# Kernel tuning notes

Hardware: AMD Instinct MI355X
Metric: run time of the kernel (lower is better)

The kernel has to match this reference:

```python
import jax, jax.numpy as jnp
import numpy as np

B, S, D, H = 2, 2048, 1024, 16
DK = D // H

def setup_inputs() -> dict:
    key = jax.random.key(0)
    ks = jax.random.split(key, 12)
    sc = 0.02
    return {
        "q": jax.random.normal(ks[0], (B, S, D), jnp.float32),
        "k": jax.random.normal(ks[1], (B, S, D), jnp.float32),
        "v": jax.random.normal(ks[2], (B, S, D), jnp.float32),
        "mask": jnp.ones((1, 1, S, S), jnp.int32),
        "w_q": jax.random.normal(ks[3], (D, D), jnp.float32) * sc,
        "b_q": jnp.zeros((D,), jnp.float32),
        "w_k": jax.random.normal(ks[4], (D, D), jnp.float32) * sc,
        "b_k": jnp.zeros((D,), jnp.float32),
        "w_v": jax.random.normal(ks[5], (D, D), jnp.float32) * sc,
        "b_v": jnp.zeros((D,), jnp.float32),
        "w_o": jax.random.normal(ks[6], (D, D), jnp.float32) * sc,
        "b_o": jnp.zeros((D,), jnp.float32),
    }

def reference(q, k, v, mask, w_q, b_q, w_k, b_k, w_v, b_v, w_o, b_o):
    # torch Linear: y = x @ W.T + b, W is [out, in]
    def lin(x, w, b):
        return jnp.einsum('bsd,ed->bse', x, w) + b
    # project and split heads -> [B, H, S, DK]
    def heads(x):
        return x.reshape(B, S, H, DK).transpose(0, 2, 1, 3)
    Q = heads(lin(q, w_q, b_q))
    K = heads(lin(k, w_k, b_k))
    V = heads(lin(v, w_v, b_v))
    scores = jnp.einsum('bhqd,bhkd->bhqk', Q, K) / jnp.sqrt(jnp.float32(DK))
    scores = jnp.where(mask == 0, jnp.float32(-1e9), scores)
    attn = jax.nn.softmax(scores, axis=-1)  # dropout p=0 -> identity
    ctx = jnp.einsum('bhqk,bhkd->bhqd', attn, V)
    ctx = ctx.transpose(0, 2, 1, 3).reshape(B, S, D)
    return lin(ctx, w_o, b_o)
```

## Files before the change

kernel.cpp:

```cpp
#include <hip/hip_runtime.h>
#include <stdint.h>


#define S_LEN 2048
#define LOG2E 1.4426950408889634f

using bf16x8 = __attribute__((ext_vector_type(8))) __bf16;
using f32x4 = __attribute__((ext_vector_type(4))) float;
using f32x16 = __attribute__((ext_vector_type(16))) float;
using u32x4 = __attribute__((ext_vector_type(4))) unsigned int;

__device__ __forceinline__ unsigned short f2bf(float x) {
  unsigned int u = __builtin_bit_cast(unsigned int, x);
  u += 0x7fffu + ((u >> 16) & 1u);
  return (unsigned short)(u >> 16);
}

__device__ __forceinline__ void gload_lds16(const void* g, void* l) {
  __builtin_amdgcn_global_load_lds(
      (const __attribute__((address_space(1))) void*)g,
      (__attribute__((address_space(3))) void*)l, 16, 0, 0);
}

__device__ __forceinline__ unsigned int cvtpk(float lo, float hi) {
  unsigned int r;
  asm("v_cvt_pk_bf16_f32 %0, %1, %2" : "=v"(r) : "v"(lo), "v"(hi));
  return r;
}

__device__ __forceinline__ bf16x8 mkfrag(float p0, float p1, float p2, float p3,
                                         float p4, float p5, float p6, float p7) {
  auto r02 = __builtin_amdgcn_permlane32_swap(cvtpk(p0, p1), cvtpk(p4, p5),
                                              false, false);
  auto r13 = __builtin_amdgcn_permlane32_swap(cvtpk(p2, p3), cvtpk(p6, p7),
                                              false, false);
  u32x4 w = {(unsigned int)r02[0], (unsigned int)r13[0], (unsigned int)r02[1],
             (unsigned int)r13[1]};
  return __builtin_bit_cast(bf16x8, w);
}

__global__ void cvt4_kernel(const float* __restrict__ s0,
                            const float* __restrict__ s1,
                            const float* __restrict__ s2,
                            const float* __restrict__ s3,
                            unsigned short* __restrict__ d0,
                            unsigned short* __restrict__ d1,
                            unsigned short* __restrict__ d2,
                            unsigned short* __restrict__ d3, int n4) {
  const int which = blockIdx.y;
  const float* src = which == 0 ? s0 : which == 1 ? s1 : which == 2 ? s2 : s3;
  unsigned short* dst = which == 0 ? d0 : which == 1 ? d1 : which == 2 ? d2 : d3;
  int i = blockIdx.x * blockDim.x + threadIdx.x;
  int stride = gridDim.x * blockDim.x;
  for (; i < n4; i += stride) {
    float4 v = ((const float4*)src)[i];
    ushort4 o;
    o.x = f2bf(v.x);
    o.y = f2bf(v.y);
    o.z = f2bf(v.z);
    o.w = f2bf(v.w);
    ((ushort4*)dst)[i] = o;
  }
}

template <bool SWAP>
__device__ __forceinline__ void qkv_body(const float* __restrict__ X,
                                         const unsigned short* __restrict__ W,
                                         const float* __restrict__ bias,
                                         unsigned short* __restrict__ dst,
                                         float scale) {
  __shared__ unsigned short As[64 * 32];
  __shared__ unsigned short Bs[128 * 32];
  const int tid = threadIdx.x;
  const int wid = tid >> 6;
  const int lane = tid & 63;
  const int l15 = lane & 15, lg = lane >> 4;
  const int bm = blockIdx.y * 64;
  const int bn = blockIdx.x * 128;
  const int wr = (wid >> 1) * 32;
  const int wc = (wid & 1) * 64;

  const f32x4 fz = {0.f, 0.f, 0.f, 0.f};
  f32x4 acc[2][4];
#pragma unroll
  for (int m = 0; m < 2; ++m)
#pragma unroll
    for (int n = 0; n < 4; ++n) acc[m][n] = fz;

  const int ar = tid >> 2, ac = (tid & 3) * 8;
  const float* Ag = X + (size_t)(bm + ar) * 1024 + ac;
  const int srow = lane >> 2, scol = (lane & 3) * 8;

  for (int kt = 0; kt < 1024; kt += 32) {
    float4 a0 = *(const float4*)(Ag + kt);
    float4 a1 = *(const float4*)(Ag + kt + 4);
    u32x4 ap = {cvtpk(a0.x, a0.y), cvtpk(a0.z, a0.w), cvtpk(a1.x, a1.y),
                cvtpk(a1.z, a1.w)};
    *(u32x4*)&As[ar * 32 + ac] = ap;
#pragma unroll
    for (int c = 0; c < 2; ++c) {
      int ch = wid * 2 + c;
      gload_lds16(W + (size_t)(bn + ch * 16 + srow) * 1024 + kt + scol,
                  Bs + ch * 512);
    }
    __syncthreads();

    bf16x8 af[2], bfr[4];
#pragma unroll
    for (int m = 0; m < 2; ++m)
      af[m] = *(const bf16x8*)&As[(wr + m * 16 + l15) * 32 + lg * 8];
#pragma unroll
    for (int n = 0; n < 4; ++n)
      bfr[n] = *(const bf16x8*)&Bs[(wc + n * 16 + l15) * 32 + lg * 8];

#pragma unroll
    for (int m = 0; m < 2; ++m)
#pragma unroll
      for (int n = 0; n < 4; ++n) {
        if (SWAP)
          acc[m][n] = __builtin_amdgcn_mfma_f32_16x16x32_bf16(
              bfr[n], af[m], acc[m][n], 0, 0, 0);
        else
          acc[m][n] = __builtin_amdgcn_mfma_f32_16x16x32_bf16(
              af[m], bfr[n], acc[m][n], 0, 0, 0);
      }
    __syncthreads();
  }

#pragma unroll
  for (int m = 0; m < 2; ++m)
#pragma unroll
    for (int n = 0; n < 4; ++n)
#pragma unroll
      for (int j = 0; j < 4; ++j) {
        float a = acc[m][n][j];
        if (SWAP) {
          int gn = bn + wc + n * 16 + lg * 4 + j;
          int gm = bm + wr + m * 16 + l15;
          float v = a + bias[gn];
          int b = gm >> 11, s = gm & 2047;
          int h = gn >> 6, dk = gn & 63;
          dst[(((size_t)(b * 16 + h)) * 64 + dk) * 2048 + s] = f2bf(v);
        } else {
          int gm = bm + wr + m * 16 + lg * 4 + j;
          int gn = bn + wc + n * 16 + l15;
          float v = (a + bias[gn]) * scale;
          int b = gm >> 11, s = gm & 2047;
          int h = gn >> 6, dk = gn & 63;
          dst[(((size_t)(b * 16 + h)) * 2048 + s) * 64 + dk] = f2bf(v);
        }
      }
}

__global__ __launch_bounds__(256) void gemm_qkv(
    const float* __restrict__ X0, const float* __restrict__ X1,
    const float* __restrict__ X2, const unsigned short* __restrict__ W0,
    const unsigned short* __restrict__ W1,
    const unsigned short* __restrict__ W2, const float* __restrict__ b0,
    const float* __restrict__ b1, const float* __restrict__ b2,
    unsigned short* __restrict__ dq, unsigned short* __restrict__ dk,
    unsigned short* __restrict__ dv) {
  const int z = blockIdx.z;
  if (z == 0)
    qkv_body<false>(X0, W0, b0, dq, 0.125f * LOG2E);
  else if (z == 1)
    qkv_body<false>(X1, W1, b1, dk, 1.0f);
  else
    qkv_body<true>(X2, W2, b2, dv, 1.0f);
}

__global__ __launch_bounds__(256) void gemm_out(
    const unsigned short* __restrict__ X, const unsigned short* __restrict__ W,
    const float* __restrict__ bias, float* __restrict__ dstF) {
  __shared__ unsigned short As[64 * 32];
  __shared__ unsigned short Bs[128 * 32];
  const int tid = threadIdx.x;
  const int wid = tid >> 6;
  const int lane = tid & 63;
  const int l15 = lane & 15, lg = lane >> 4;
  const int bm = blockIdx.y * 64;
  const int bn = blockIdx.x * 128;
  const int wr = (wid >> 1) * 32;
  const int wc = (wid & 1) * 64;

  const f32x4 fz = {0.f, 0.f, 0.f, 0.f};
  f32x4 acc[2][4];
#pragma unroll
  for (int m = 0; m < 2; ++m)
#pragma unroll
    for (int n = 0; n < 4; ++n) acc[m][n] = fz;

  const int srow = lane >> 2, scol = (lane & 3) * 8;

  for (int kt = 0; kt < 1024; kt += 32) {
    gload_lds16(X + (size_t)(bm + wid * 16 + srow) * 1024 + kt + scol,
                As + wid * 512);
#pragma unroll
    for (int c = 0; c < 2; ++c) {
      int ch = wid * 2 + c;
      gload_lds16(W + (size_t)(bn + ch * 16 + srow) * 1024 + kt + scol,
                  Bs + ch * 512);
    }
    __syncthreads();

    bf16x8 af[2], bfr[4];
#pragma unroll
    for (int m = 0; m < 2; ++m)
      af[m] = *(const bf16x8*)&As[(wr + m * 16 + l15) * 32 + lg * 8];
#pragma unroll
    for (int n = 0; n < 4; ++n)
      bfr[n] = *(const bf16x8*)&Bs[(wc + n * 16 + l15) * 32 + lg * 8];

#pragma unroll
    for (int m = 0; m < 2; ++m)
#pragma unroll
      for (int n = 0; n < 4; ++n)
        acc[m][n] = __builtin_amdgcn_mfma_f32_16x16x32_bf16(af[m], bfr[n],
                                                            acc[m][n], 0, 0, 0);
    __syncthreads();
  }

#pragma unroll
  for (int m = 0; m < 2; ++m)
#pragma unroll
    for (int n = 0; n < 4; ++n)
#pragma unroll
      for (int j = 0; j < 4; ++j) {
        int gm = bm + wr + m * 16 + lg * 4 + j;
        int gn = bn + wc + n * 16 + l15;
        dstF[(size_t)gm * 1024 + gn] = acc[m][n][j] + bias[gn];
      }
}

__global__ __launch_bounds__(256) void attn_kernel(
    const unsigned short* __restrict__ Q,
    const unsigned short* __restrict__ K,
    const unsigned short* __restrict__ VT,
    unsigned short* __restrict__ CTX) {
  const int orig = blockIdx.x;
  const int wg = (orig & 7) * 64 + (orig >> 3);
  const int bh = wg >> 4;
  const int qb = wg & 15;
  const int tid = threadIdx.x;
  const int w = tid >> 6;
  const int lane = tid & 63;
  const int l31 = lane & 31;
  const int hi = lane >> 5;
  const int q0 = qb * 128 + w * 32;

  __shared__ __align__(16) unsigned short Ks[3][64][64];
  __shared__ __align__(16) unsigned short Vs[3][64][64];
  __shared__ float ls[4][32];

  const unsigned short* Qg = Q + ((size_t)bh * S_LEN + q0) * 64;
  const unsigned short* Kg = K + (size_t)bh * S_LEN * 64;
  const unsigned short* Vg = VT + (size_t)bh * 64 * S_LEN;

  bf16x8 qf[4];
#pragma unroll
  for (int kc = 0; kc < 4; ++kc)
    qf[kc] = *(const bf16x8*)&Qg[l31 * 64 + kc * 16 + hi * 8];

  const int srow = lane >> 3;
  const int sslot = (lane & 7) ^ srow;

#define STAGE(buf, kt)                                                         \
  {                                                                            \
    gload_lds16(Kg + ((size_t)((kt) + w * 16 + srow)) * 64 + sslot * 8,        \
                &Ks[buf][w * 16][0]);                                          \
    gload_lds16(Kg + ((size_t)((kt) + w * 16 + 8 + srow)) * 64 + sslot * 8,    \
                &Ks[buf][w * 16 + 8][0]);                                      \
    gload_lds16(Vg + ((size_t)(w * 16 + srow)) * S_LEN + (kt) + sslot * 8,     \
                &Vs[buf][w * 16][0]);                                          \
    gload_lds16(Vg + ((size_t)(w * 16 + 8 + srow)) * S_LEN + (kt) + sslot * 8, \
                &Vs[buf][w * 16 + 8][0]);                                      \
  }

  f32x16 O0 = {}, O1 = {};
  float m = -1e30f, lsum = 0.f;

  STAGE(0, 0)
  STAGE(1, 64)
  int cur = 0;

  for (int t = 0; t < 32; ++t) {
    if (t < 31) {
      asm volatile("s_waitcnt vmcnt(4)\n\ts_barrier" ::: "memory");
    } else {
      asm volatile("s_waitcnt vmcnt(0)\n\ts_barrier" ::: "memory");
    }
    if (t < 30) {
      int nb = cur >= 1 ? cur - 1 : cur + 2;
      STAGE(nb, (t + 2) * 64)
    }

    f32x16 s0 = {}, s1 = {};
    __builtin_amdgcn_s_setprio(1);
#pragma unroll
    for (int kc = 0; kc < 4; ++kc) {
      const int col = ((kc * 2 + hi) ^ (l31 & 7)) * 8;
      bf16x8 kf0 = *(const bf16x8*)&Ks[cur][l31][col];
      bf16x8 kf1 = *(const bf16x8*)&Ks[cur][32 + l31][col];
      s0 = __builtin_amdgcn_mfma_f32_32x32x16_bf16(kf0, qf[kc], s0, 0, 0, 0);
      s1 = __builtin_amdgcn_mfma_f32_32x32x16_bf16(kf1, qf[kc], s1, 0, 0, 0);
    }
    __builtin_amdgcn_s_setprio(0);

    float tmax[8];
#pragma unroll
    for (int i = 0; i < 8; ++i)
      tmax[i] = fmaxf(fmaxf(s0[i], s0[i + 8]), fmaxf(s1[i], s1[i + 8]));
    float pm = fmaxf(fmaxf(fmaxf(tmax[0], tmax[1]), fmaxf(tmax[2], tmax[3])),
                     fmaxf(fmaxf(tmax[4], tmax[5]), fmaxf(tmax[6], tmax[7])));
    pm = fmaxf(pm, __shfl_xor(pm, 32, 64));

    if (!__all(pm - m <= 8.0f)) {
      float mn = fmaxf(m, pm);
      float al = exp2f(m - mn);
      m = mn;
      lsum *= al;
      ls[w][l31] = al;
#pragma unroll
      for (int r = 0; r < 16; ++r) {
        float a = ls[w][(r & 3) + 8 * (r >> 2) + 4 * hi];
        O0[r] *= a;
        O1[r] *= a;
      }
    }

#pragma unroll
    for (int r = 0; r < 16; ++r) {
      s0[r] = exp2f(s0[r] - m);
      s1[r] = exp2f(s1[r] - m);
    }
    float sa = 0.f, sb = 0.f, sc = 0.f, sd = 0.f;
#pragma unroll
    for (int r = 0; r < 4; ++r) {
      sa += s0[r];
      sb += s0[r + 4];
      sc += s0[r + 8];
      sd += s0[r + 12];
      sa += s1[r];
      sb += s1[r + 4];
      sc += s1[r + 8];
      sd += s1[r + 12];
    }
    float ts = (sa + sb) + (sc + sd);
    ts += __shfl_xor(ts, 32, 64);
    lsum += ts;

    bf16x8 pa0 = mkfrag(s0[0], s0[1], s0[2], s0[3], s0[4], s0[5], s0[6], s0[7]);
    bf16x8 pa1 =
        mkfrag(s0[8], s0[9], s0[10], s0[11], s0[12], s0[13], s0[14], s0[15]);
    bf16x8 pa2 = mkfrag(s1[0], s1[1], s1[2], s1[3], s1[4], s1[5], s1[6], s1[7]);
    bf16x8 pa3 =
        mkfrag(s1[8], s1[9], s1[10], s1[11], s1[12], s1[13], s1[14], s1[15]);

    __builtin_amdgcn_s_setprio(1);
#pragma unroll
    for (int kc = 0; kc < 4; ++kc) {
      const int col = ((kc * 2 + hi) ^ (l31 & 7)) * 8;
      bf16x8 v0 = *(const bf16x8*)&Vs[cur][l31][col];
      bf16x8 v1 = *(const bf16x8*)&Vs[cur][32 + l31][col];
      bf16x8 pa = (kc == 0) ? pa0 : (kc == 1) ? pa1 : (kc == 2) ? pa2 : pa3;
      O0 = __builtin_amdgcn_mfma_f32_32x32x16_bf16(pa, v0, O0, 0, 0, 0);
      O1 = __builtin_amdgcn_mfma_f32_32x32x16_bf16(pa, v1, O1, 0, 0, 0);
    }
    __builtin_amdgcn_s_setprio(0);

    cur = cur == 2 ? 0 : cur + 1;
  }

  ls[w][l31] = lsum;
  const int b = bh >> 4, h = bh & 15;
#pragma unroll
  for (int r = 0; r < 16; ++r) {
    int qr = (r & 3) + 8 * (r >> 2) + 4 * hi;
    float inv = __builtin_amdgcn_rcpf(ls[w][qr]);
    size_t base = ((size_t)b * S_LEN + q0 + qr) * 1024 + h * 64;
    CTX[base + l31] = f2bf(O0[r] * inv);
    CTX[base + 32 + l31] = f2bf(O1[r] * inv);
  }
#undef STAGE
}

extern "C" void kernel_launch(void* const* d_in, const int* in_sizes, int n_in,
                              void* d_out, int out_size, void* d_ws,
                              size_t ws_size, hipStream_t stream) {
  const float* q = (const float*)d_in[0];
  const float* k = (const float*)d_in[1];
  const float* v = (const float*)d_in[2];
  const float* wq = (const float*)d_in[4];
  const float* bq = (const float*)d_in[5];
  const float* wk = (const float*)d_in[6];
  const float* bk = (const float*)d_in[7];
  const float* wv = (const float*)d_in[8];
  const float* bv = (const float*)d_in[9];
  const float* wo = (const float*)d_in[10];
  const float* bo = (const float*)d_in[11];
  float* out = (float*)d_out;

  const size_t NTOK = 4096 * 1024;
  unsigned short* ws = (unsigned short*)d_ws;
  unsigned short* wqb = ws;
  unsigned short* wkb = wqb + 1048576;
  unsigned short* wvb = wkb + 1048576;
  unsigned short* wob = wvb + 1048576;
  unsigned short* Qp = wob + 1048576;
  unsigned short* Kp = Qp + NTOK;
  unsigned short* Vt = Kp + NTOK;
  unsigned short* CTX = Vt + NTOK;

  cvt4_kernel<<<dim3(256, 4), 256, 0, stream>>>(wq, wk, wv, wo, wqb, wkb, wvb,
                                                wob, 262144);

  gemm_qkv<<<dim3(8, 64, 3), 256, 0, stream>>>(q, k, v, wqb, wkb, wvb, bq, bk,
                                               bv, Qp, Kp, Vt);

  attn_kernel<<<512, 256, 0, stream>>>(Qp, Kp, Vt, CTX);

  gemm_out<<<dim3(8, 64), 256, 0, stream>>>(CTX, wob, bo, out);
}
```

Measured before the change: 166.9 us.

## Enlarge GEMM tiles to 128x128 and remap blocks per XCD for L2 locality

Both projection GEMMs now share one templated body with 128x128 output tiles, with each wave computing 64x64 (4x4 MFMA fragments) instead of 32x64. This halves the block count and doubles the A-tile reuse per loaded B tile. Block indices are also remapped so each XCD handles contiguous row panels, keeping weight and activation tiles resident in that XCD's L2. The trade-off is more accumulator registers per thread and fewer blocks in flight (768 and 256), which lowers occupancy and can hurt latency hiding in the single-buffered loop.

After: 172.8 us. 3.6% more time.

```diff
diff --git a/kernel.cpp b/kernel.cpp
--- a/kernel.cpp
+++ b/kernel.cpp
@@ -63,40 +63,51 @@
   }
 }
 
-template <bool SWAP>
-__device__ __forceinline__ void qkv_body(const float* __restrict__ X,
-                                         const unsigned short* __restrict__ W,
-                                         const float* __restrict__ bias,
-                                         unsigned short* __restrict__ dst,
-                                         float scale) {
-  __shared__ unsigned short As[64 * 32];
+template <int APATH, int OMODE>
+__device__ __forceinline__ void gemm128_body(
+    const void* Xv, const unsigned short* __restrict__ W,
+    const float* __restrict__ bias, unsigned short* __restrict__ dstB,
+    float* __restrict__ dstF, float scale, int tx, int ty) {
+  __shared__ unsigned short As[128 * 32];
   __shared__ unsigned short Bs[128 * 32];
   const int tid = threadIdx.x;
-  const int wid = tid >> 6;
-  const int lane = tid & 63;
+  const int wid = tid >> 6, lane = tid & 63;
   const int l15 = lane & 15, lg = lane >> 4;
-  const int bm = blockIdx.y * 64;
-  const int bn = blockIdx.x * 128;
-  const int wr = (wid >> 1) * 32;
-  const int wc = (wid & 1) * 64;
+  const int bm = ty * 128, bn = tx * 128;
+  const int wr = (wid >> 1) * 64, wc = (wid & 1) * 64;
 
   const f32x4 fz = {0.f, 0.f, 0.f, 0.f};
-  f32x4 acc[2][4];
-#pragma unroll
-  for (int m = 0; m < 2; ++m)
+  f32x4 acc[4][4];
+#pragma unroll
+  for (int m = 0; m < 4; ++m)
 #pragma unroll
     for (int n = 0; n < 4; ++n) acc[m][n] = fz;
 
-  const int ar = tid >> 2, ac = (tid & 3) * 8;
-  const float* Ag = X + (size_t)(bm + ar) * 1024 + ac;
   const int srow = lane >> 2, scol = (lane & 3) * 8;
+  const int ar = tid >> 1, ac = (tid & 1) * 16;
+  const float* Af = (const float*)Xv + (size_t)(bm + ar) * 1024 + ac;
+  const unsigned short* Ab = (const unsigned short*)Xv;
 
   for (int kt = 0; kt < 1024; kt += 32) {
-    float4 a0 = *(const float4*)(Ag + kt);
-    float4 a1 = *(const float4*)(Ag + kt + 4);
-    u32x4 ap = {cvtpk(a0.x, a0.y), cvtpk(a0.z, a0.w), cvtpk(a1.x, a1.y),
-                cvtpk(a1.z, a1.w)};
-    *(u32x4*)&As[ar * 32 + ac] = ap;
+    if (APATH == 0) {
+      float4 a0 = *(const float4*)(Af + kt);
+      float4 a1 = *(const float4*)(Af + kt + 4);
+      float4 a2 = *(const float4*)(Af + kt + 8);
+      float4 a3 = *(const float4*)(Af + kt + 12);
+      u32x4 p0 = {cvtpk(a0.x, a0.y), cvtpk(a0.z, a0.w), cvtpk(a1.x, a1.y),
+                  cvtpk(a1.z, a1.w)};
+      u32x4 p1 = {cvtpk(a2.x, a2.y), cvtpk(a2.z, a2.w), cvtpk(a3.x, a3.y),
+                  cvtpk(a3.z, a3.w)};
+      *(u32x4*)&As[ar * 32 + ac] = p0;
+      *(u32x4*)&As[ar * 32 + ac + 8] = p1;
+    } else {
+#pragma unroll
+      for (int c = 0; c < 2; ++c) {
+        int ch = wid * 2 + c;
+        gload_lds16(Ab + (size_t)(bm + ch * 16 + srow) * 1024 + kt + scol,
+                    As + ch * 512);
+      }
+    }
 #pragma unroll
     for (int c = 0; c < 2; ++c) {
       int ch = wid * 2 + c;
@@ -105,49 +116,53 @@
     }
     __syncthreads();
 
-    bf16x8 af[2], bfr[4];
-#pragma unroll
-    for (int m = 0; m < 2; ++m)
+    bf16x8 af[4], bf[4];
+#pragma unroll
+    for (int m = 0; m < 4; ++m)
       af[m] = *(const bf16x8*)&As[(wr + m * 16 + l15) * 32 + lg * 8];
 #pragma unroll
     for (int n = 0; n < 4; ++n)
-      bfr[n] = *(const bf16x8*)&Bs[(wc + n * 16 + l15) * 32 + lg * 8];
-
-#pragma unroll
-    for (int m = 0; m < 2; ++m)
+      bf[n] = *(const bf16x8*)&Bs[(wc + n * 16 + l15) * 32 + lg * 8];
+
+#pragma unroll
+    for (int m = 0; m < 4; ++m)
 #pragma unroll
       for (int n = 0; n < 4; ++n) {
-        if (SWAP)
-          acc[m][n] = __builtin_amdgcn_mfma_f32_16x16x32_bf16(
-              bfr[n], af[m], acc[m][n], 0, 0, 0);
+        if (OMODE == 2)
+          acc[m][n] = __builtin_amdgcn_mfma_f32_16x16x32_bf16(bf[n], af[m],
+                                                              acc[m][n], 0, 0, 0);
         else
-          acc[m][n] = __builtin_amdgcn_mfma_f32_16x16x32_bf16(
-              af[m], bfr[n], acc[m][n], 0, 0, 0);
+          acc[m][n] = __builtin_amdgcn_mfma_f32_16x16x32_bf16(af[m], bf[n],
+                                                              acc[m][n], 0, 0, 0);
       }
     __syncthreads();
   }
 
 #pragma unroll
-  for (int m = 0; m < 2; ++m)
+  for (int m = 0; m < 4; ++m)
 #pragma unroll
     for (int n = 0; n < 4; ++n)
 #pragma unroll
       for (int j = 0; j < 4; ++j) {
         float a = acc[m][n][j];
-        if (SWAP) {
+        if (OMODE == 3) {
+          int gm = bm + wr + m * 16 + lg * 4 + j;
+          int gn = bn + wc + n * 16 + l15;
+          dstF[(size_t)gm * 1024 + gn] = a + bias[gn];
+        } else if (OMODE == 2) {
           int gn = bn + wc + n * 16 + lg * 4 + j;
           int gm = bm + wr + m * 16 + l15;
           float v = a + bias[gn];
           int b = gm >> 11, s = gm & 2047;
           int h = gn >> 6, dk = gn & 63;
-          dst[(((size_t)(b * 16 + h)) * 64 + dk) * 2048 + s] = f2bf(v);
+          dstB[(((size_t)(b * 16 + h)) * 64 + dk) * 2048 + s] = f2bf(v);
         } else {
           int gm = bm + wr + m * 16 + lg * 4 + j;
           int gn = bn + wc + n * 16 + l15;
           float v = (a + bias[gn]) * scale;
           int b = gm >> 11, s = gm & 2047;
           int h = gn >> 6, dk = gn & 63;
-          dst[(((size_t)(b * 16 + h)) * 2048 + s) * 64 + dk] = f2bf(v);
+          dstB[(((size_t)(b * 16 + h)) * 2048 + s) * 64 + dk] = f2bf(v);
         }
       }
 }
@@ -160,76 +175,27 @@
     const float* __restrict__ b1, const float* __restrict__ b2,
     unsigned short* __restrict__ dq, unsigned short* __restrict__ dk,
     unsigned short* __restrict__ dv) {
-  const int z = blockIdx.z;
+  const int lin = blockIdx.x + 8 * (blockIdx.y + 32 * blockIdx.z);
+  const int xcd = lin & 7, v = lin >> 3;
+  const int panel = xcd * 12 + (v >> 3);
+  const int tx = v & 7;
+  const int z = panel >> 5, ty = panel & 31;
   if (z == 0)
-    qkv_body<false>(X0, W0, b0, dq, 0.125f * LOG2E);
+    gemm128_body<0, 0>(X0, W0, b0, dq, nullptr, 0.125f * LOG2E, tx, ty);
   else if (z == 1)
-    qkv_body<false>(X1, W1, b1, dk, 1.0f);
+    gemm128_body<0, 0>(X1, W1, b1, dk, nullptr, 1.0f, tx, ty);
   else
-    qkv_body<true>(X2, W2, b2, dv, 1.0f);
+    gemm128_body<0, 2>(X2, W2, b2, dv, nullptr, 1.0f, tx, ty);
 }
 
 __global__ __launch_bounds__(256) void gemm_out(
     const unsigned short* __restrict__ X, const unsigned short* __restrict__ W,
     const float* __restrict__ bias, float* __restrict__ dstF) {
-  __shared__ unsigned short As[64 * 32];
-  __shared__ unsigned short Bs[128 * 32];
-  const int tid = threadIdx.x;
-  const int wid = tid >> 6;
-  const int lane = tid & 63;
-  const int l15 = lane & 15, lg = lane >> 4;
-  const int bm = blockIdx.y * 64;
-  const int bn = blockIdx.x * 128;
-  const int wr = (wid >> 1) * 32;
-  const int wc = (wid & 1) * 64;
-
-  const f32x4 fz = {0.f, 0.f, 0.f, 0.f};
-  f32x4 acc[2][4];
-#pragma unroll
-  for (int m = 0; m < 2; ++m)
-#pragma unroll
-    for (int n = 0; n < 4; ++n) acc[m][n] = fz;
-
-  const int srow = lane >> 2, scol = (lane & 3) * 8;
-
-  for (int kt = 0; kt < 1024; kt += 32) {
-    gload_lds16(X + (size_t)(bm + wid * 16 + srow) * 1024 + kt + scol,
-                As + wid * 512);
-#pragma unroll
-    for (int c = 0; c < 2; ++c) {
-      int ch = wid * 2 + c;
-      gload_lds16(W + (size_t)(bn + ch * 16 + srow) * 1024 + kt + scol,
-                  Bs + ch * 512);
-    }
-    __syncthreads();
-
-    bf16x8 af[2], bfr[4];
-#pragma unroll
-    for (int m = 0; m < 2; ++m)
-      af[m] = *(const bf16x8*)&As[(wr + m * 16 + l15) * 32 + lg * 8];
-#pragma unroll
-    for (int n = 0; n < 4; ++n)
-      bfr[n] = *(const bf16x8*)&Bs[(wc + n * 16 + l15) * 32 + lg * 8];
-
-#pragma unroll
-    for (int m = 0; m < 2; ++m)
-#pragma unroll
-      for (int n = 0; n < 4; ++n)
-        acc[m][n] = __builtin_amdgcn_mfma_f32_16x16x32_bf16(af[m], bfr[n],
-                                                            acc[m][n], 0, 0, 0);
-    __syncthreads();
-  }
-
-#pragma unroll
-  for (int m = 0; m < 2; ++m)
-#pragma unroll
-    for (int n = 0; n < 4; ++n)
-#pragma unroll
-      for (int j = 0; j < 4; ++j) {
-        int gm = bm + wr + m * 16 + lg * 4 + j;
-        int gn = bn + wc + n * 16 + l15;
-        dstF[(size_t)gm * 1024 + gn] = acc[m][n][j] + bias[gn];
-      }
+  const int lin = blockIdx.x + 8 * blockIdx.y;
+  const int xcd = lin & 7, v = lin >> 3;
+  const int panel = xcd * 4 + (v >> 3);
+  const int tx = v & 7;
+  gemm128_body<1, 3>(X, W, bias, nullptr, dstF, 1.0f, tx, panel);
 }
 
 __global__ __launch_bounds__(256) void attn_kernel(
@@ -414,10 +380,10 @@
   cvt4_kernel<<<dim3(256, 4), 256, 0, stream>>>(wq, wk, wv, wo, wqb, wkb, wvb,
                                                 wob, 262144);
 
-  gemm_qkv<<<dim3(8, 64, 3), 256, 0, stream>>>(q, k, v, wqb, wkb, wvb, bq, bk,
+  gemm_qkv<<<dim3(8, 32, 3), 256, 0, stream>>>(q, k, v, wqb, wkb, wvb, bq, bk,
                                                bv, Qp, Kp, Vt);
 
   attn_kernel<<<512, 256, 0, stream>>>(Qp, Kp, Vt, CTX);
 
-  gemm_out<<<dim3(8, 64), 256, 0, stream>>>(CTX, wob, bo, out);
-}
+  gemm_out<<<dim3(8, 32), 256, 0, stream>>>(CTX, wob, bo, out);
+}
```
